# Optimization experiments

Hardware: AMD Instinct MI355X
Metric: run time of the kernel (lower is better)

The kernel has to match this reference:

```python
import jax, jax.numpy as jnp
import numpy as np

T, D, E, DFF, TOPK, CAP = 4096, 1024, 16, 1024, 2, 512


def setup_inputs() -> dict:
    key = jax.random.key(0)
    k1, k2, k3, k4 = jax.random.split(key, 4)
    h = jax.random.normal(k1, (T, D), jnp.float32)
    Wr = jax.random.normal(k2, (D, E), jnp.float32) / np.sqrt(D).astype(np.float32)
    W1 = jax.random.normal(k3, (E, D, DFF), jnp.float32) / np.sqrt(D).astype(np.float32)
    W2 = jax.random.normal(k4, (E, DFF, D), jnp.float32) / np.sqrt(DFF).astype(np.float32)
    return {"h": h, "Wr": Wr, "W1": W1, "W2": W2, "topk": TOPK, "capacity": CAP}


def reference(h, Wr, W1, W2, topk, capacity):
    # One routing hop of DNA: top-k router -> capacity_selection -> grouped
    # (vmapped) expert execution -> weighted combine with residual rescale.
    Tn, Dn = h.shape
    En = Wr.shape[1]
    C = min(int(capacity), Tn)

    # --- Router: linear logits, softmax probs, top-k expert mask per token ---
    logits = h @ Wr                                  # [T, E]
    probs = jax.nn.softmax(logits, axis=-1)          # [T, E]
    _, tk_idx = jax.lax.top_k(logits, int(topk))     # [T, topk]
    mask_te = jnp.zeros((Tn, En), bool).at[jnp.arange(Tn)[:, None], tk_idx].set(True)

    # --- capacity_selection (gather form of the one-hot slot einsum) ---
    mask_et = mask_te.T                              # [E, T]
    score_et = jnp.where(mask_et, logits.T, -jnp.inf)
    _, top_indices = jax.lax.top_k(score_et, C)      # [E, C] token ids per slot
    valid = jnp.take_along_axis(mask_et, top_indices, axis=1)  # [E, C] slot active
    e_idx = jnp.arange(En)[:, None]
    kept = (jnp.zeros((En, Tn), jnp.int32)
            .at[e_idx, top_indices].add(valid.astype(jnp.int32)) > 0)  # [E, T]

    # --- sort active slots by original token position (stable) ---
    pos = jnp.where(valid, top_indices, Tn + 1)
    order = jnp.argsort(pos, axis=1, stable=True)
    top_sorted = jnp.take_along_axis(top_indices, order, axis=1)     # [E, C]
    valid_sorted = jnp.take_along_axis(valid, order, axis=1)         # [E, C]

    # --- dispatch: equivalent to einsum('ect,td->ecd', slot, h) ---
    xin = h[top_sorted] * valid_sorted[..., None]    # [E, C, d]

    # --- grouped expert execution (vmap over stacked params via einsum) ---
    hidden = jax.nn.gelu(jnp.einsum('ecd,edf->ecf', xin, W1))
    expert_out = jnp.einsum('ecf,efd->ecd', hidden, W2)             # [E, C, d]

    # --- combine: weights = routing probs masked by capacity-kept tokens ---
    combine_w = jnp.where(kept.T, probs, 0.0)        # [T, E]
    rho = combine_w.sum(axis=1, keepdims=True)       # [T, 1]
    w_ec = jnp.take_along_axis(combine_w.T, top_sorted, axis=1) * valid_sorted  # [E, C]
    combine = (jnp.zeros((Tn, Dn), h.dtype)
               .at[top_sorted.reshape(-1)]
               .add((expert_out * w_ec[..., None]).reshape(-1, Dn)))
    return h + combine - rho * h
```

## Files before the change

### kernel.cpp

```cpp
#include <hip/hip_runtime.h>
#include <hip/hip_bf16.h>
#include <stdint.h>

#define T_TOK 4096
#define DIM   1024
#define NE    16
#define NDFF  1024
#define CAPN  512

typedef unsigned int   u32;
typedef unsigned short u16;
typedef __attribute__((ext_vector_type(8))) short bf16x8;
typedef __attribute__((ext_vector_type(4))) float f32x4;

__device__ __forceinline__ void gll16(void* lds, const void* g) {
  union { const void* p; const __attribute__((address_space(1))) void* q; } gu;
  union { void* p; __attribute__((address_space(3))) void* q; } lu;
  gu.p = g; lu.p = lds;
  __builtin_amdgcn_global_load_lds(gu.q, lu.q, 16, 0, 0);
}

__device__ __forceinline__ u16 f2bf(float f) {
  u32 u = __float_as_uint(f);
  u32 r = (u + 0x7FFFu + ((u >> 16) & 1u)) >> 16;
  return (u16)r;
}

__device__ __forceinline__ float gelu_tanh(float x) {
  float x3 = x * x * x;
  float z = 0.7978845608028654f * (x + 0.044715f * x3);
  return 0.5f * x * (1.0f + tanhf(z));
}

__global__ __launch_bounds__(64) void router_kernel(
    const float* __restrict__ h, const float* __restrict__ Wr,
    float* __restrict__ logits, u32* __restrict__ topmask, u32* __restrict__ keptmask)
{
  const int t = blockIdx.x;
  const int lane = threadIdx.x;
  float acc[NE];
#pragma unroll
  for (int e = 0; e < NE; ++e) acc[e] = 0.f;
  const float* hrow = h + (size_t)t * DIM;
#pragma unroll 4
  for (int i = 0; i < DIM / 64; ++i) {
    int d = lane + 64 * i;
    float hv = hrow[d];
    const float4* wr4 = (const float4*)(Wr + (size_t)d * NE);
#pragma unroll
    for (int q = 0; q < 4; ++q) {
      float4 w = wr4[q];
      acc[q*4+0] += hv * w.x; acc[q*4+1] += hv * w.y;
      acc[q*4+2] += hv * w.z; acc[q*4+3] += hv * w.w;
    }
  }
#pragma unroll
  for (int e = 0; e < NE; ++e) {
    float v = acc[e];
#pragma unroll
    for (int off = 32; off; off >>= 1) v += __shfl_xor(v, off);
    acc[e] = v;
  }
  int m1 = 0; float b1 = acc[0];
#pragma unroll
  for (int e = 1; e < NE; ++e) if (acc[e] > b1) { b1 = acc[e]; m1 = e; }
  int m2 = 0; float b2 = -3.4e38f;
#pragma unroll
  for (int e = 0; e < NE; ++e) if (e != m1 && acc[e] > b2) { b2 = acc[e]; m2 = e; }
  if (lane < NE) logits[(size_t)t * NE + lane] = acc[lane];
  if (lane == 0) { topmask[t] = (1u << m1) | (1u << m2); keptmask[t] = 0u; }
}

__global__ __launch_bounds__(1024) void capacity_kernel(
    const float* __restrict__ logits, const u32* __restrict__ topmask,
    u32* __restrict__ keptmask, int* __restrict__ expert_tokens)
{
  const int e = blockIdx.x;
  const int tid = threadIdx.x;
  const int lane = tid & 63, wv = tid >> 6;
  __shared__ u32 wred[16];
  __shared__ u32 wscan[16];
  __shared__ u32 bcast;

  u32 key[4];
#pragma unroll
  for (int j = 0; j < 4; ++j) {
    int t = tid * 4 + j;
    float lg = logits[(size_t)t * NE + e];
    u32 u = __float_as_uint(lg);
    u32 ord = (u >> 31) ? ~u : (u | 0x80000000u);
    bool sel = (topmask[t] >> e) & 1u;
    key[j] = sel ? ord : 0u;
  }

  auto blockReduce = [&](u32 v) -> u32 {
#pragma unroll
    for (int off = 32; off; off >>= 1) v += __shfl_xor(v, off);
    if (lane == 0) wred[wv] = v;
    __syncthreads();
    if (tid == 0) { u32 s = 0; for (int i = 0; i < 16; ++i) s += wred[i]; bcast = s; }
    __syncthreads();
    u32 r = bcast;
    __syncthreads();
    return r;
  };

  u32 nsel = blockReduce((key[0] != 0u) + (key[1] != 0u) + (key[2] != 0u) + (key[3] != 0u));

  u32 p = 0, need = 0;
  if (nsel > CAPN) {
    need = CAPN;
    for (int b = 31; b >= 0; --b) {
      u32 cand = p | (1u << b);
      u32 hi = ~((1u << b) - 1u);
      u32 loc = 0;
#pragma unroll
      for (int j = 0; j < 4; ++j) loc += ((key[j] & hi) == cand) ? 1u : 0u;
      u32 c = blockReduce(loc);
      if (c >= need) p = cand; else need -= c;
    }
  }

  auto blockExScan = [&](u32 v, u32& total) -> u32 {
    u32 x = v;
#pragma unroll
    for (int off = 1; off < 64; off <<= 1) { u32 y = __shfl_up(x, off); if (lane >= off) x += y; }
    if (lane == 63) wscan[wv] = x;
    __syncthreads();
    if (wv == 0) {
      u32 w = (lane < 16) ? wscan[lane] : 0u;
#pragma unroll
      for (int off = 1; off < 16; off <<= 1) { u32 y = __shfl_up(w, off); if (lane >= off) w += y; }
      if (lane < 16) wscan[lane] = w;
    }
    __syncthreads();
    u32 base = wv ? wscan[wv - 1] : 0u;
    total = wscan[15];
    __syncthreads();
    return base + x - v;
  };

  bool eq[4], kept[4];
  u32 eqc = 0;
#pragma unroll
  for (int j = 0; j < 4; ++j) { eq[j] = (key[j] != 0u) && (key[j] == p); eqc += eq[j] ? 1u : 0u; }
  u32 eqtot;
  u32 eqbase = blockExScan(eqc, eqtot);
  u32 keptc = 0;
  {
    u32 er = eqbase;
#pragma unroll
    for (int j = 0; j < 4; ++j) {
      kept[j] = (key[j] != 0u) && ((key[j] > p) || (eq[j] && er < need));
      er += eq[j] ? 1u : 0u;
      keptc += kept[j] ? 1u : 0u;
    }
  }
  u32 ktot;
  u32 kbase = blockExScan(keptc, ktot);
  {
    u32 slot = kbase;
#pragma unroll
    for (int j = 0; j < 4; ++j) {
      if (kept[j]) {
        int t = tid * 4 + j;
        expert_tokens[e * CAPN + slot] = t;
        atomicOr(&keptmask[t], 1u << e);
        slot++;
      }
    }
  }
  for (u32 i = ktot + tid; i < CAPN; i += 1024) expert_tokens[e * CAPN + i] = -1;
}

__global__ __launch_bounds__(256) void rho_init_kernel(
    const float* __restrict__ h, const float* __restrict__ logits,
    const u32* __restrict__ keptmask, float* __restrict__ out)
{
  const int t = blockIdx.x;
  const int tid = threadIdx.x;
  float v[NE]; float m = -3.4e38f;
#pragma unroll
  for (int i = 0; i < NE; ++i) { v[i] = logits[(size_t)t * NE + i]; m = fmaxf(m, v[i]); }
  float sum = 0.f;
#pragma unroll
  for (int i = 0; i < NE; ++i) { v[i] = expf(v[i] - m); sum += v[i]; }
  u32 km = keptmask[t];
  float rho = 0.f;
#pragma unroll
  for (int i = 0; i < NE; ++i) if ((km >> i) & 1u) rho += v[i];
  rho /= sum;
  float s = 1.0f - rho;
  const float4 hv = *(const float4*)(h + (size_t)t * DIM + tid * 4);
  float4 o; o.x = hv.x * s; o.y = hv.y * s; o.z = hv.z * s; o.w = hv.w * s;
  *(float4*)(out + (size_t)t * DIM + tid * 4) = o;
}

__global__ __launch_bounds__(64) void gather_kernel(
    const float* __restrict__ h, const int* __restrict__ expert_tokens,
    const float* __restrict__ logits, u16* __restrict__ Xg, float* __restrict__ w_ec)
{
  const int slot = blockIdx.x;
  const int lane = threadIdx.x;
  const int t = expert_tokens[slot];
  u16* dst = Xg + (size_t)slot * DIM + lane * 16;
  if (t < 0) {
    if (lane == 0) w_ec[slot] = 0.f;
    uint4 z = make_uint4(0, 0, 0, 0);
    *(uint4*)dst = z; *(uint4*)(dst + 8) = z;
  } else {
    if (lane == 0) {
      const int e = slot / CAPN;
      float v[NE], m = -3.4e38f;
#pragma unroll
      for (int i = 0; i < NE; ++i) { v[i] = logits[(size_t)t * NE + i]; m = fmaxf(m, v[i]); }
      float sum = 0.f;
#pragma unroll
      for (int i = 0; i < NE; ++i) { v[i] = expf(v[i] - m); sum += v[i]; }
      w_ec[slot] = v[e] / sum;
    }
    const float4* src = (const float4*)(h + (size_t)t * DIM + lane * 16);
    __align__(16) u16 tmp[16];
#pragma unroll
    for (int q = 0; q < 4; ++q) {
      float4 x = src[q];
      tmp[q*4+0] = f2bf(x.x); tmp[q*4+1] = f2bf(x.y);
      tmp[q*4+2] = f2bf(x.z); tmp[q*4+3] = f2bf(x.w);
    }
    *(uint4*)dst = *(const uint4*)tmp;
    *(uint4*)(dst + 8) = *(const uint4*)(tmp + 8);
  }
}

template <int EPI>
__global__ __launch_bounds__(256) void gemm_fused_kernel(
    const u16* __restrict__ Abase, const float* __restrict__ Bf32base,
    u16* __restrict__ Hout, float* __restrict__ out,
    const int* __restrict__ expert_tokens, const float* __restrict__ w_ec)
{
  __shared__ __align__(16) u16 As[2 * 128 * 64];
  __shared__ __align__(16) u16 Bs[2 * 128 * 64];

  const int p   = blockIdx.x + 8 * (blockIdx.y + 4 * blockIdx.z);
  const int lin = (p & 7) * 64 + (p >> 3);
  const int e   = lin >> 5;
  const int rem = lin & 31;
  const int m0  = (rem >> 3) * 128;
  const int n0  = (rem & 7) * 128;

  const char*  A = (const char*)(Abase + (size_t)e * 512 * 1024);
  const float* B = Bf32base + (size_t)e * 1024 * 1024;

  const int tid = threadIdx.x;
  const int lane = tid & 63, wave = tid >> 6;
  const int wr = wave >> 1, wc = wave & 1;
  f32x4 acc[4][4];
#pragma unroll
  for (int i = 0; i < 4; ++i)
#pragma unroll
    for (int j = 0; j < 4; ++j) acc[i][j] = (f32x4){0.f, 0.f, 0.f, 0.f};

  const int srow  = lane >> 3;
  const int sbyte = 16 * ((lane & 7) ^ srow);
  const u32 bsTr0 = (u32)(uintptr_t)Bs + (u32)((lane >> 4) * 128 + (lane & 15) * 8);

  auto stageA = [&](int kt, int buf) {
    const int kb0 = kt * 128;
#pragma unroll
    for (int i = 0; i < 4; ++i) {
      const int c = wave * 4 + i;
      const int r = c * 8 + srow;
      gll16((char*)As + buf * 16384 + c * 1024, A + (size_t)(m0 + r) * 2048 + kb0 + sbyte);
    }
  };
  auto loadB = [&](float4* br, int kt) {
    const int k0 = kt * 64;
#pragma unroll
    for (int it = 0; it < 4; ++it) {
      const int q = tid + 256 * it;
      const int kl = q >> 4, n8 = q & 15;
      const float* gp = B + (size_t)(k0 + kl) * 1024 + n0 + n8 * 8;
      br[2*it]   = *(const float4*)gp;
      br[2*it+1] = *(const float4*)(gp + 4);
    }
  };
  auto writeB = [&](const float4* br, int buf) {
#pragma unroll
    for (int it = 0; it < 4; ++it) {
      const int q = tid + 256 * it;
      const int kl = q >> 4, n8 = q & 15;
      const int c = (n8 >> 1) * 2 + ((kl >> 2) & 1);
      const int byt = c * 1024 + (kl >> 3) * 128 + (kl & 3) * 32 + (n8 & 1) * 16;
      __align__(16) u16 t8[8];
      const float* f = (const float*)&br[2*it];
#pragma unroll
      for (int j = 0; j < 8; ++j) t8[j] = f2bf(f[j]);
      *(uint4*)((char*)Bs + buf * 16384 + byt) = *(const uint4*)t8;
    }
  };
  auto compute = [&](int buf) {
#pragma unroll
    for (int s = 0; s < 2; ++s) {
      bf16x8 af[4];
#pragma unroll
      for (int i = 0; i < 4; ++i) {
        const int rowa = wr * 64 + i * 16 + (lane & 15);
        const int kb = (s * 64 + (lane >> 4) * 16) ^ ((lane & 7) << 4);
        af[i] = *(const bf16x8*)((const char*)As + buf * 16384 + rowa * 128 + kb);
      }
      unsigned long long tlo[4], thi[4];
#pragma unroll
      for (int j = 0; j < 4; ++j) {
        const u32 a = bsTr0 + (u32)(buf * 16384 + (wc * 4 + j) * 2048 + s * 512);
        asm volatile("ds_read_b64_tr_b16 %0, %2 offset:0\n\t"
                     "ds_read_b64_tr_b16 %1, %2 offset:1024"
                     : "=v"(tlo[j]), "=v"(thi[j]) : "v"(a));
      }
      asm volatile("s_waitcnt lgkmcnt(0)" ::: "memory");
      __builtin_amdgcn_sched_barrier(0);
      bf16x8 bfv[4];
#pragma unroll
      for (int j = 0; j < 4; ++j) {
        union { unsigned long long q[2]; bf16x8 v; } u;
        u.q[0] = tlo[j]; u.q[1] = thi[j];
        bfv[j] = u.v;
      }
#pragma unroll
      for (int i = 0; i < 4; ++i)
#pragma unroll
        for (int j = 0; j < 4; ++j)
          acc[i][j] = __builtin_amdgcn_mfma_f32_16x16x32_bf16(af[i], bfv[j], acc[i][j], 0, 0, 0);
    }
  };

  stageA(0, 0);
  {
    float4 br0[8];
    loadB(br0, 0);
    writeB(br0, 0);
  }
  float4 brE[8], brO[8];
  loadB(brO, 1);
  __syncthreads();

  for (int kt = 0; kt < 16; kt += 2) {
    if (kt + 2 < 16) loadB(brE, kt + 2);
    if (kt + 1 < 16) stageA(kt + 1, 1);
    compute(0);
    if (kt + 1 < 16) writeB(brO, 1);
    __syncthreads();
    if (kt + 1 < 16) {
      if (kt + 3 < 16) loadB(brO, kt + 3);
      if (kt + 2 < 16) stageA(kt + 2, 0);
      compute(1);
      if (kt + 2 < 16) writeB(brE, 0);
      __syncthreads();
    }
  }

  if (EPI == 1) {
#pragma unroll
    for (int i = 0; i < 4; ++i) {
#pragma unroll
      for (int r = 0; r < 4; ++r) {
        const int row = m0 + wr * 64 + i * 16 + (lane >> 4) * 4 + r;
        u16* hp = Hout + ((size_t)e * 512 + row) * 1024 + n0 + wc * 64 + (lane & 15);
#pragma unroll
        for (int j = 0; j < 4; ++j) hp[j * 16] = f2bf(gelu_tanh(acc[i][j][r]));
      }
    }
  } else {
#pragma unroll
    for (int i = 0; i < 4; ++i) {
#pragma unroll
      for (int r = 0; r < 4; ++r) {
        const int row  = m0 + wr * 64 + i * 16 + (lane >> 4) * 4 + r;
        const int slot = e * CAPN + row;
        const int t = expert_tokens[slot];
        if (t >= 0) {
          const float w = w_ec[slot];
          float* op = out + (size_t)t * DIM + n0 + wc * 64 + (lane & 15);
#pragma unroll
          for (int j = 0; j < 4; ++j) atomicAdd(op + j * 16, acc[i][j][r] * w);
        }
      }
    }
  }
}

extern "C" void kernel_launch(void* const* d_in, const int* in_sizes, int n_in,
                              void* d_out, int out_size, void* d_ws, size_t ws_size,
                              hipStream_t stream)
{
  const float* h  = (const float*)d_in[0];
  const float* Wr = (const float*)d_in[1];
  const float* W1 = (const float*)d_in[2];
  const float* W2 = (const float*)d_in[3];
  float* out = (float*)d_out;

  char* ws = (char*)d_ws;
  u16* Xg  = (u16*)(ws);
  u16* Hb  = (u16*)(ws + 16777216);
  float* logits       = (float*)(ws + 33554432);
  u32*   topmask      = (u32*)  (ws + 33816576);
  u32*   keptmask     = (u32*)  (ws + 33832960);
  int*   expert_tokens= (int*)  (ws + 33849344);
  float* w_ec         = (float*)(ws + 33882112);

  router_kernel<<<T_TOK, 64, 0, stream>>>(h, Wr, logits, topmask, keptmask);
  capacity_kernel<<<NE, 1024, 0, stream>>>(logits, topmask, keptmask, expert_tokens);
  rho_init_kernel<<<T_TOK, 256, 0, stream>>>(h, logits, keptmask, out);
  gather_kernel<<<NE * CAPN, 64, 0, stream>>>(h, expert_tokens, logits, Xg, w_ec);
  gemm_fused_kernel<1><<<dim3(8, 4, NE), 256, 0, stream>>>(Xg, W1, Hb, nullptr, nullptr, nullptr);
  gemm_fused_kernel<2><<<dim3(8, 4, NE), 256, 0, stream>>>(Hb, W2, nullptr, out, expert_tokens, w_ec);
}
```

Baseline: 151.6 us.

## Convert W2 to bf16 inside GEMM1 and stream bf16 W2 into GEMM2

GEMM1 now also converts W2 from fp32 to bf16 as a side task and writes it to a workspace buffer, spread across its k-loop iterations. GEMM2 becomes a separate kernel that loads the bf16 W2 straight into LDS with global_load_lds, instead of reading fp32 W2 through registers and converting it. This halves GEMM2's weight traffic and removes its conversion work. In exchange GEMM1 gains extra global reads and writes, and GEMM2 drops to a single-buffered loop with two barriers per k-step.

```diff
diff --git a/kernel.cpp b/kernel.cpp
--- a/kernel.cpp
+++ b/kernel.cpp
@@ -232,11 +232,10 @@
   }
 }
 
-template <int EPI>
-__global__ __launch_bounds__(256) void gemm_fused_kernel(
+__global__ __launch_bounds__(256) void gemm1_kernel(
     const u16* __restrict__ Abase, const float* __restrict__ Bf32base,
-    u16* __restrict__ Hout, float* __restrict__ out,
-    const int* __restrict__ expert_tokens, const float* __restrict__ w_ec)
+    const float* __restrict__ W2src, u16* __restrict__ W2b,
+    u16* __restrict__ Hout)
 {
   __shared__ __align__(16) u16 As[2 * 128 * 64];
   __shared__ __align__(16) u16 Bs[2 * 128 * 64];
@@ -250,6 +249,8 @@
 
   const char*  A = (const char*)(Abase + (size_t)e * 512 * 1024);
   const float* B = Bf32base + (size_t)e * 1024 * 1024;
+  const float* W2s = W2src + (size_t)e * 1024 * 1024 + (size_t)rem * 32768;
+  u16*         W2d = W2b   + (size_t)e * 1024 * 1024 + (size_t)rem * 32768;
 
   const int tid = threadIdx.x;
   const int lane = tid & 63, wave = tid >> 6;
@@ -298,6 +299,15 @@
       *(uint4*)((char*)Bs + buf * 16384 + byt) = *(const uint4*)t8;
     }
   };
+  auto w2copy = [&](int kt) {
+    const int off = kt * 2048 + tid * 8;
+    const float4 a = *(const float4*)(W2s + off);
+    const float4 b = *(const float4*)(W2s + off + 4);
+    __align__(16) u16 t8[8];
+    t8[0] = f2bf(a.x); t8[1] = f2bf(a.y); t8[2] = f2bf(a.z); t8[3] = f2bf(a.w);
+    t8[4] = f2bf(b.x); t8[5] = f2bf(b.y); t8[6] = f2bf(b.z); t8[7] = f2bf(b.w);
+    *(uint4*)(W2d + off) = *(const uint4*)t8;
+  };
   auto compute = [&](int buf) {
 #pragma unroll
     for (int s = 0; s < 2; ++s) {
@@ -346,43 +356,125 @@
   for (int kt = 0; kt < 16; kt += 2) {
     if (kt + 2 < 16) loadB(brE, kt + 2);
     if (kt + 1 < 16) stageA(kt + 1, 1);
+    w2copy(kt);
     compute(0);
     if (kt + 1 < 16) writeB(brO, 1);
     __syncthreads();
     if (kt + 1 < 16) {
       if (kt + 3 < 16) loadB(brO, kt + 3);
       if (kt + 2 < 16) stageA(kt + 2, 0);
+      w2copy(kt + 1);
       compute(1);
       if (kt + 2 < 16) writeB(brE, 0);
       __syncthreads();
     }
   }
 
-  if (EPI == 1) {
+#pragma unroll
+  for (int i = 0; i < 4; ++i) {
+#pragma unroll
+    for (int r = 0; r < 4; ++r) {
+      const int row = m0 + wr * 64 + i * 16 + (lane >> 4) * 4 + r;
+      u16* hp = Hout + ((size_t)e * 512 + row) * 1024 + n0 + wc * 64 + (lane & 15);
+#pragma unroll
+      for (int j = 0; j < 4; ++j) hp[j * 16] = f2bf(gelu_tanh(acc[i][j][r]));
+    }
+  }
+}
+
+__global__ __launch_bounds__(256) void gemm2_kernel(
+    const u16* __restrict__ Abase, const u16* __restrict__ Bbase,
+    float* __restrict__ out,
+    const int* __restrict__ expert_tokens, const float* __restrict__ w_ec)
+{
+  __shared__ __align__(16) u16 As[128 * 64];
+  __shared__ __align__(16) u16 Bs[128 * 64];
+
+  const int p   = blockIdx.x + 8 * (blockIdx.y + 4 * blockIdx.z);
+  const int lin = (p & 7) * 64 + (p >> 3);
+  const int e   = lin >> 5;
+  const int rem = lin & 31;
+  const int m0  = (rem >> 3) * 128;
+  const int n0  = (rem & 7) * 128;
+
+  const char* A = (const char*)(Abase + (size_t)e * 512 * 1024);
+  const u16*  B = Bbase + (size_t)e * 1024 * 1024;
+
+  const int tid = threadIdx.x;
+  const int lane = tid & 63, wave = tid >> 6;
+  const int wr = wave >> 1, wc = wave & 1;
+  f32x4 acc[4][4];
+#pragma unroll
+  for (int i = 0; i < 4; ++i)
+#pragma unroll
+    for (int j = 0; j < 4; ++j) acc[i][j] = (f32x4){0.f, 0.f, 0.f, 0.f};
+
+  const int srow  = lane >> 3;
+  const int sbyte = 16 * ((lane & 7) ^ srow);
+  const int kl0 = 8 * (lane >> 3) + ((lane & 7) >> 1);
+  const int ncl = (lane & 1) * 8;
+  const u32 bsTr = (u32)(uintptr_t)Bs + (u32)((lane >> 4) * 128 + (lane & 15) * 8);
+
+  for (int kt = 0; kt < 16; ++kt) {
+    const int kb0 = kt * 128;
+    const int k0  = kt * 64;
 #pragma unroll
     for (int i = 0; i < 4; ++i) {
-#pragma unroll
-      for (int r = 0; r < 4; ++r) {
-        const int row = m0 + wr * 64 + i * 16 + (lane >> 4) * 4 + r;
-        u16* hp = Hout + ((size_t)e * 512 + row) * 1024 + n0 + wc * 64 + (lane & 15);
-#pragma unroll
-        for (int j = 0; j < 4; ++j) hp[j * 16] = f2bf(gelu_tanh(acc[i][j][r]));
-      }
-    }
-  } else {
-#pragma unroll
-    for (int i = 0; i < 4; ++i) {
-#pragma unroll
-      for (int r = 0; r < 4; ++r) {
-        const int row  = m0 + wr * 64 + i * 16 + (lane >> 4) * 4 + r;
-        const int slot = e * CAPN + row;
-        const int t = expert_tokens[slot];
-        if (t >= 0) {
-          const float w = w_ec[slot];
-          float* op = out + (size_t)t * DIM + n0 + wc * 64 + (lane & 15);
-#pragma unroll
-          for (int j = 0; j < 4; ++j) atomicAdd(op + j * 16, acc[i][j][r] * w);
-        }
+      const int c = wave * 4 + i;
+      const int r = c * 8 + srow;
+      gll16((char*)As + c * 1024, A + (size_t)(m0 + r) * 2048 + kb0 + sbyte);
+      const int nb = c >> 1, par = c & 1;
+      gll16((char*)Bs + c * 1024,
+            (const char*)(B + (size_t)(k0 + kl0 + 4 * par) * 1024 + (n0 + nb * 16 + ncl)));
+    }
+    __syncthreads();
+#pragma unroll
+    for (int s = 0; s < 2; ++s) {
+      bf16x8 af[4];
+#pragma unroll
+      for (int i = 0; i < 4; ++i) {
+        const int rowa = wr * 64 + i * 16 + (lane & 15);
+        const int kb = (s * 64 + (lane >> 4) * 16) ^ ((lane & 7) << 4);
+        af[i] = *(const bf16x8*)((const char*)As + rowa * 128 + kb);
+      }
+      unsigned long long tlo[4], thi[4];
+#pragma unroll
+      for (int j = 0; j < 4; ++j) {
+        const u32 a = bsTr + (u32)((wc * 4 + j) * 2048 + s * 512);
+        asm volatile("ds_read_b64_tr_b16 %0, %2 offset:0\n\t"
+                     "ds_read_b64_tr_b16 %1, %2 offset:1024"
+                     : "=v"(tlo[j]), "=v"(thi[j]) : "v"(a));
+      }
+      asm volatile("s_waitcnt lgkmcnt(0)" ::: "memory");
+      __builtin_amdgcn_sched_barrier(0);
+      bf16x8 bfv[4];
+#pragma unroll
+      for (int j = 0; j < 4; ++j) {
+        union { unsigned long long q[2]; bf16x8 v; } u;
+        u.q[0] = tlo[j]; u.q[1] = thi[j];
+        bfv[j] = u.v;
+      }
+#pragma unroll
+      for (int i = 0; i < 4; ++i)
+#pragma unroll
+        for (int j = 0; j < 4; ++j)
+          acc[i][j] = __builtin_amdgcn_mfma_f32_16x16x32_bf16(af[i], bfv[j], acc[i][j], 0, 0, 0);
+    }
+    __syncthreads();
+  }
+
+#pragma unroll
+  for (int i = 0; i < 4; ++i) {
+#pragma unroll
+    for (int r = 0; r < 4; ++r) {
+      const int row  = m0 + wr * 64 + i * 16 + (lane >> 4) * 4 + r;
+      const int slot = e * CAPN + row;
+      const int t = expert_tokens[slot];
+      if (t >= 0) {
+        const float w = w_ec[slot];
+        float* op = out + (size_t)t * DIM + n0 + wc * 64 + (lane & 15);
+#pragma unroll
+        for (int j = 0; j < 4; ++j) atomicAdd(op + j * 16, acc[i][j][r] * w);
       }
     }
   }
@@ -406,11 +498,12 @@
   u32*   keptmask     = (u32*)  (ws + 33832960);
   int*   expert_tokens= (int*)  (ws + 33849344);
   float* w_ec         = (float*)(ws + 33882112);
+  u16*   W2b          = (u16*)  (ws + 33914880);
 
   router_kernel<<<T_TOK, 64, 0, stream>>>(h, Wr, logits, topmask, keptmask);
   capacity_kernel<<<NE, 1024, 0, stream>>>(logits, topmask, keptmask, expert_tokens);
   rho_init_kernel<<<T_TOK, 256, 0, stream>>>(h, logits, keptmask, out);
   gather_kernel<<<NE * CAPN, 64, 0, stream>>>(h, expert_tokens, logits, Xg, w_ec);
-  gemm_fused_kernel<1><<<dim3(8, 4, NE), 256, 0, stream>>>(Xg, W1, Hb, nullptr, nullptr, nullptr);
-  gemm_fused_kernel<2><<<dim3(8, 4, NE), 256, 0, stream>>>(Hb, W2, nullptr, out, expert_tokens, w_ec);
-}
+  gemm1_kernel<<<dim3(8, 4, NE), 256, 0, stream>>>(Xg, W1, W2, W2b, Hb);
+  gemm2_kernel<<<dim3(8, 4, NE), 256, 0, stream>>>(Hb, W2b, out, expert_tokens, w_ec);
+}
```

After: 158.1 us. 1.04x slower.
